# Performance work log

Measured on AMD Instinct MI355X. Metric: run time of the kernel, lower is better.

Reference implementation:

```python
import jax, jax.numpy as jnp
import numpy as np

N_NODES = 100000
N_EDGES = 1600000
IN_DIM = 128
OUT_DIM = 128
ALPHA = 0.2  # leaky relu negative slope
EPS = 9e-15


def setup_inputs() -> dict:
    key = jax.random.key(0)
    k1, k2, k3, k4, k5 = jax.random.split(key, 5)
    x = jax.random.normal(k1, (N_NODES, IN_DIM), dtype=jnp.float32)
    src = jax.random.randint(k2, (N_EDGES,), 0, N_NODES)
    dst = jax.random.randint(k3, (N_EDGES,), 0, N_NODES)
    edge_index = jnp.stack([src, dst]).astype(jnp.int64)
    # xavier-normal-ish params
    W = jax.random.normal(k4, (IN_DIM, OUT_DIM), dtype=jnp.float32) * (1.414 * np.sqrt(2.0 / (IN_DIM + OUT_DIM)))
    attn = jax.random.normal(k5, (1, 2 * OUT_DIM), dtype=jnp.float32) * (1.414 * np.sqrt(2.0 / (1 + 2 * OUT_DIM)))
    return {"x": x, "edge_index": edge_index, "W": W, "attn": attn}


def reference(x, edge_index, W, attn):
    N = x.shape[0]
    h = x @ W  # [N, out_dim]
    d = h.shape[1]
    a_src, a_dst = attn[0, :d], attn[0, d:]
    src, dst = edge_index[0], edge_index[1]
    # attn @ cat(h[src], h[dst]) == (h @ a_src)[src] + (h @ a_dst)[dst]
    values = (h @ a_src)[src] + (h @ a_dst)[dst]  # [E]
    e_a = jnp.where(values > 0, values, ALPHA * values)  # leaky relu
    edge_e = jnp.exp(e_a - jnp.max(e_a))  # [E]
    rowsum = jax.ops.segment_sum(edge_e, src, num_segments=N)  # [N]
    h_prime = jax.ops.segment_sum(edge_e[:, None] * h[dst], src, num_segments=N)  # [N, d]
    h_prime = h_prime / (rowsum[:, None] + EPS)
    return jax.nn.elu(h_prime)
```

## Files before the change

kernel.cpp:

```cpp
#include <hip/hip_runtime.h>
#include <hip/hip_bf16.h>
#include <stdint.h>


#define NN 100000
#define NE 1600000
#define DIM 128
#define ALPHA_ 0.2f
#define EPS_ 9e-15f

#define NB 1563
#define CHUNK 4096
#define NPART 391
#define NGEMM 1564
#define SDEG 56

typedef short bf16x8 __attribute__((ext_vector_type(8)));
typedef float floatx4 __attribute__((ext_vector_type(4)));

static __device__ __forceinline__ float bflo(unsigned u){ return __uint_as_float(u << 16); }
static __device__ __forceinline__ float bfhi(unsigned u){ return __uint_as_float(u & 0xFFFF0000u); }
static __device__ __forceinline__ float bfs(unsigned short s){ return __uint_as_float((unsigned)s << 16); }
static __device__ __forceinline__ unsigned short f2bf(float f){
  unsigned b = __float_as_uint(f);
  unsigned r = (b + 0x7FFFu + ((b >> 16) & 1u)) >> 16;
  return (unsigned short)r;
}
static __device__ __forceinline__ unsigned short f2bf_rhu(float f){
  return (unsigned short)((__float_as_uint(f) + 0x8000u) >> 16);
}
static __device__ __forceinline__ unsigned fkey(float f){
  unsigned u = __float_as_uint(f);
  return (u & 0x80000000u) ? ~u : (u | 0x80000000u);
}
static __device__ __forceinline__ float dkey(unsigned k){
  unsigned u = (k & 0x80000000u) ? (k ^ 0x80000000u) : ~k;
  return __uint_as_float(u);
}

__global__ __launch_bounds__(256) void k_init(const unsigned short* W, const unsigned* EI,
                                              const unsigned short* attn, int* flags,
                                              unsigned short* attnb, unsigned short* Wt){
  __shared__ int sh_f, sh_e;
  int b = blockIdx.x, tid = threadIdx.x;
  if (b == 0){
    if (tid == 0){ sh_f = 0; sh_e = 0; }
    __syncthreads();
    for (int i = tid; i < 1024; i += 256){
      unsigned u = W[i];
      if (((u >> 7) & 0xFF) >= 0x85) sh_f = 1;
    }
    int any = 0;
    for (int k = tid; k < 2048; k += 256) any |= EI[2 * k + 1];
    atomicOr(&sh_e, any);
    __syncthreads();
    if (tid == 0){ flags[0] = sh_f; flags[1] = (sh_e == 0) ? 1 : 0; }
    __syncthreads();
    attnb[tid] = sh_f ? f2bf(((const float*)attn)[tid]) : attn[tid];
  } else {
    if (tid == 0) sh_f = 0;
    __syncthreads();
    for (int i = tid; i < 1024; i += 256){
      unsigned u = W[i];
      if (((u >> 7) & 0xFF) >= 0x85) sh_f = 1;
    }
    __syncthreads();
    int i = (b - 1) * 256 + tid;
    int k = i >> 7, n = i & 127;
    unsigned short v = sh_f ? f2bf(((const float*)W)[i]) : ((const unsigned short*)W)[i];
    Wt[n * DIM + k] = v;
  }
}

static __device__ __forceinline__ void load_edge(const int* EI, int e64, int e,
                                                 int& s, int& d){
  if (e64){
    const long long* E64 = (const long long*)EI;
    s = (int)E64[e];
    d = (int)E64[NE + e];
  } else {
    s = EI[e];
    d = EI[NE + e];
  }
}

static __device__ __forceinline__ void gemm_path(int gid, char* smem,
                                                 const void* X, const int* flags,
                                                 const unsigned short* Wt,
                                                 const unsigned short* attnb,
                                                 unsigned short* H, float* s1, float* s2,
                                                 float* gmax1, float* gmax2){
  char* wlds = smem;
  float* sm1 = (float*)(smem + 16384);
  float* sm2 = sm1 + 4;
  int tid = threadIdx.x;
  int wid = tid >> 6, lane = tid & 63;
  int m = lane & 15, q = lane >> 4;
  int rb = gid * 64 + wid * 16;
  int row = rb + m;
  bool rok = row < NN;
  int fx32 = flags[0];

  floatx4 acc[8];
  #pragma unroll
  for (int t = 0; t < 8; t++){ acc[t][0]=0.f; acc[t][1]=0.f; acc[t][2]=0.f; acc[t][3]=0.f; }

  for (int hk = 0; hk < 2; hk++){
    float4 f0, f1, f2, f3;
    bf16x8 a0, a1;
    if (rok){
      if (fx32){
        const float* xr = (const float*)X + (size_t)row * DIM + hk * 64 + q * 8;
        f0 = ((const float4*)xr)[0];
        f1 = ((const float4*)xr)[1];
        f2 = ((const float4*)(xr + 32))[0];
        f3 = ((const float4*)(xr + 32))[1];
      } else {
        const unsigned short* xr = (const unsigned short*)X + (size_t)row * DIM + hk * 64 + q * 8;
        a0 = *(const bf16x8*)xr;
        a1 = *(const bf16x8*)(xr + 32);
      }
    }
    for (int j = tid; j < 1024; j += 256){
      int wr = j >> 3, c = j & 7;
      uint4 v = ((const uint4*)Wt)[wr * 16 + hk * 8 + c];
      *(uint4*)(wlds + ((wr * 8 + (c ^ (wr & 7))) << 4)) = v;
    }
    __syncthreads();
    bf16x8 fr[2];
    #pragma unroll
    for (int j = 0; j < 8; j++){ fr[0][j] = 0; fr[1][j] = 0; }
    if (rok){
      if (fx32){
        fr[0][0] = (short)f2bf_rhu(f0.x); fr[0][1] = (short)f2bf_rhu(f0.y);
        fr[0][2] = (short)f2bf_rhu(f0.z); fr[0][3] = (short)f2bf_rhu(f0.w);
        fr[0][4] = (short)f2bf_rhu(f1.x); fr[0][5] = (short)f2bf_rhu(f1.y);
        fr[0][6] = (short)f2bf_rhu(f1.z); fr[0][7] = (short)f2bf_rhu(f1.w);
        fr[1][0] = (short)f2bf_rhu(f2.x); fr[1][1] = (short)f2bf_rhu(f2.y);
        fr[1][2] = (short)f2bf_rhu(f2.z); fr[1][3] = (short)f2bf_rhu(f2.w);
        fr[1][4] = (short)f2bf_rhu(f3.x); fr[1][5] = (short)f2bf_rhu(f3.y);
        fr[1][6] = (short)f2bf_rhu(f3.z); fr[1][7] = (short)f2bf_rhu(f3.w);
      } else {
        fr[0] = a0; fr[1] = a1;
      }
    }
    #pragma unroll
    for (int ki2 = 0; ki2 < 2; ki2++){
      #pragma unroll
      for (int t = 0; t < 8; t++){
        int rowb = t * 16 + m;
        bf16x8 bfr = *(const bf16x8*)(wlds + ((rowb * 8 + ((ki2 * 4 + q) ^ (m & 7))) << 4));
        acc[t] = __builtin_amdgcn_mfma_f32_16x16x32_bf16(fr[ki2], bfr, acc[t], 0, 0, 0);
      }
    }
    __syncthreads();
  }

  float as[8], ad[8];
  #pragma unroll
  for (int t = 0; t < 8; t++){
    as[t] = bfs(attnb[t * 16 + m]);
    ad[t] = bfs(attnb[DIM + t * 16 + m]);
  }
  float lm1 = -3.0e38f, lm2 = -3.0e38f;
  #pragma unroll
  for (int r = 0; r < 4; r++){
    int grow = rb + q * 4 + r;
    float p1 = 0.f, p2 = 0.f;
    #pragma unroll
    for (int t = 0; t < 8; t++){ p1 += acc[t][r] * as[t]; p2 += acc[t][r] * ad[t]; }
    #pragma unroll
    for (int off = 1; off < 16; off <<= 1){
      p1 += __shfl_xor(p1, off);
      p2 += __shfl_xor(p2, off);
    }
    if (grow < NN){
      if (m == 0){ s1[grow] = p1; s2[grow] = p2; }
      lm1 = fmaxf(lm1, p1); lm2 = fmaxf(lm2, p2);
    }
  }
  #pragma unroll
  for (int off = 32; off; off >>= 1){
    lm1 = fmaxf(lm1, __shfl_xor(lm1, off));
    lm2 = fmaxf(lm2, __shfl_xor(lm2, off));
  }
  if (lane == 0){ sm1[wid] = lm1; sm2[wid] = lm2; }
  __syncthreads();
  if (tid == 0){
    gmax1[gid] = fmaxf(fmaxf(sm1[0], sm1[1]), fmaxf(sm1[2], sm1[3]));
    gmax2[gid] = fmaxf(fmaxf(sm2[0], sm2[1]), fmaxf(sm2[2], sm2[3]));
  }

  char* wb = wlds + wid * 4096;
  #pragma unroll
  for (int r = 0; r < 4; r++){
    int trow = q * 4 + r;
    #pragma unroll
    for (int t = 0; t < 8; t++){
      int col = t * 16 + m;
      int boff = trow * 256 + (((((col >> 3) ^ trow) & 15)) << 4) + ((col & 7) << 1);
      *(unsigned short*)(wb + boff) = f2bf(acc[t][r]);
    }
  }
  __syncthreads();
  int lrow = lane >> 2;
  int grow2 = rb + lrow;
  #pragma unroll
  for (int u = 0; u < 4; u++){
    int c = u * 4 + (lane & 3);
    uint4 v = *(const uint4*)(wb + lrow * 256 + (((c ^ lrow) & 15) << 4));
    if (grow2 < NN) *(uint4*)(H + (size_t)grow2 * DIM + c * 8) = v;
  }
}

static __device__ __forceinline__ void part_path(int pid, char* smem,
                                                 const int* EI, const int* flags,
                                                 unsigned* dir, unsigned* sout_g){
  unsigned* sout = (unsigned*)smem;
  int* hist = (int*)(smem + 16384);
  int tid = threadIdx.x;
  int e0 = pid * CHUNK;
  int nmy = NE - e0; if (nmy > CHUNK) nmy = CHUNK;
  int e64 = flags[1];

  for (int i = tid; i < NB; i += 256) hist[i] = 0;
  __syncthreads();

  unsigned ent[16]; int bv[16];
  #pragma unroll
  for (int i = 0; i < 16; i++){
    int idx = tid + i * 256;
    if (idx < nmy){
      int s, d;
      load_edge(EI, e64, e0 + idx, s, d);
      ent[i] = ((unsigned)(s & 63) << 17) | (unsigned)d;
      bv[i] = s >> 6;
      atomicAdd(&hist[bv[i]], 1);
    } else {
      ent[i] = 0u; bv[i] = -1;
    }
  }
  __syncthreads();

  if (tid < 64){
    int carry = 0;
    for (int rr = 0; rr < (NB + 63) / 64; rr++){
      int idx = rr * 64 + tid;
      int v = (idx < NB) ? hist[idx] : 0;
      int x = v;
      #pragma unroll
      for (int off = 1; off < 64; off <<= 1){
        int y = __shfl_up(x, off);
        if (tid >= off) x += y;
      }
      if (idx < NB) hist[idx] = x - v + carry;
      carry += __shfl(x, 63);
    }
    if (tid == 0) hist[NB] = carry;
  }
  __syncthreads();

  for (int t = tid; t < NB; t += 256){
    unsigned ls = (unsigned)hist[t];
    unsigned len = (unsigned)(hist[t + 1] - hist[t]);
    dir[(size_t)pid * NB + t] = (ls << 16) | len;
  }
  __syncthreads();

  #pragma unroll
  for (int i = 0; i < 16; i++){
    if (bv[i] >= 0){
      int p = atomicAdd(&hist[bv[i]], 1);
      sout[p] = ent[i];
    }
  }
  __syncthreads();

  for (int i = tid * 4; i < nmy; i += 1024)
    *(uint4*)(sout_g + e0 + i) = *(const uint4*)(sout + i);
}

__global__ __launch_bounds__(256, 6) void k_main(const void* X, const int* EI,
                                                 const int* flags,
                                                 const unsigned short* Wt,
                                                 const unsigned short* attnb,
                                                 unsigned short* H, float* s1, float* s2,
                                                 float* gmax1, float* gmax2,
                                                 unsigned* dir, unsigned* sout_g){
  __shared__ char smem[22656];
  int bid = blockIdx.x;
  int T = bid / 5, r = bid % 5;
  if (r == 4){
    part_path(T, smem, EI, flags, dir, sout_g);
  } else {
    gemm_path(T * 4 + r, smem, X, flags, Wt, attnb, H, s1, s2, gmax1, gmax2);
  }
}

__global__ __launch_bounds__(256) void k_aux(const float* gmax1, const float* gmax2,
                                             unsigned* keys, const unsigned* dir,
                                             unsigned* dir_t){
  int b = blockIdx.x, tid = threadIdx.x;
  if (b == 0){
    float a = -3.0e38f, bb = -3.0e38f;
    for (int i = tid; i < NGEMM; i += 256){
      a = fmaxf(a, gmax1[i]);
      bb = fmaxf(bb, gmax2[i]);
    }
    #pragma unroll
    for (int off = 32; off; off >>= 1){
      a = fmaxf(a, __shfl_xor(a, off));
      bb = fmaxf(bb, __shfl_xor(bb, off));
    }
    __shared__ float m1[4], m2[4];
    int lane = tid & 63, wid = tid >> 6;
    if (lane == 0){ m1[wid] = a; m2[wid] = bb; }
    __syncthreads();
    if (tid == 0){
      keys[0] = fkey(fmaxf(fmaxf(m1[0], m1[1]), fmaxf(m1[2], m1[3])));
      keys[1] = fkey(fmaxf(fmaxf(m2[0], m2[1]), fmaxf(m2[2], m2[3])));
    }
  } else {
    __shared__ unsigned tile[64][65];
    int tb = b - 1;
    int tc = tb % 25;
    int tr = tb / 25;
    int r0 = tr * 64, c0 = tc * 64;
    int cc = tid & 63;
    for (int rr = tid >> 6; rr < 64; rr += 4){
      int gp = r0 + rr, gB = c0 + cc;
      unsigned v = 0;
      if (gp < NPART && gB < NB) v = dir[(size_t)gp * NB + gB];
      tile[rr][cc] = v;
    }
    __syncthreads();
    for (int rr = tid >> 6; rr < 64; rr += 4){
      int gB = c0 + rr, gp = r0 + cc;
      if (gB < NB && gp < NPART)
        dir_t[(size_t)gB * NPART + gp] = tile[cc][rr];
    }
  }
}

__global__ __launch_bounds__(256) void k_sbagg(const unsigned* dir_t, const unsigned* sout_g,
                                               const float* s1, const float* s2,
                                               const unsigned* keys,
                                               const unsigned short* H, float* out){
  __shared__ int lcnt[64];
  __shared__ int llist[64][SDEG];
  int B = blockIdx.x;
  int tid = threadIdx.x;
  if (tid < 64) lcnt[tid] = 0;
  __syncthreads();
  for (int p = tid; p < NPART; p += 256){
    unsigned dv = dir_t[(size_t)B * NPART + p];
    int len = (int)(dv & 0xFFFFu);
    if (len){
      const unsigned* sp = sout_g + (size_t)p * CHUNK + (dv >> 16);
      for (int j = 0; j < len; j++){
        unsigned ent = sp[j];
        int sl = ent >> 17;
        int pos = atomicAdd(&lcnt[sl], 1);
        if (pos < SDEG) llist[sl][pos] = ent & 0x1FFFF;
      }
    }
  }
  __syncthreads();
  float V = dkey(keys[0]) + dkey(keys[1]);
  float M = V > 0.f ? V : ALPHA_ * V;
  int wid = tid >> 6, lane = tid & 63;
  const unsigned* h2 = (const unsigned*)H;
  for (int sl = wid; sl < 64; sl += 4){
    int srcn = B * 64 + sl;
    if (srcn >= NN) break;
    int deg = lcnt[sl]; if (deg > SDEG) deg = SDEG;
    float s1n = s1[srcn];
    int pd = 0; float pw = 0.f;
    if (lane < deg){
      pd = llist[sl][lane];
      float v = s1n + s2[pd];
      float va = v > 0.f ? v : ALPHA_ * v;
      pw = __expf(va - M);
    }
    float a0 = 0.f, a1 = 0.f, wsum = 0.f;
    int j = 0;
    for (; j + 4 <= deg; j += 4){
      int d0 = __shfl(pd, j), d1 = __shfl(pd, j + 1), d2 = __shfl(pd, j + 2), d3 = __shfl(pd, j + 3);
      float w0 = __shfl(pw, j), w1 = __shfl(pw, j + 1), w2 = __shfl(pw, j + 2), w3 = __shfl(pw, j + 3);
      unsigned v0 = h2[d0 * 64 + lane];
      unsigned v1 = h2[d1 * 64 + lane];
      unsigned v2 = h2[d2 * 64 + lane];
      unsigned v3 = h2[d3 * 64 + lane];
      a0 += w0 * bflo(v0) + w1 * bflo(v1) + w2 * bflo(v2) + w3 * bflo(v3);
      a1 += w0 * bfhi(v0) + w1 * bfhi(v1) + w2 * bfhi(v2) + w3 * bfhi(v3);
      wsum += (w0 + w1) + (w2 + w3);
    }
    for (; j < deg; j++){
      int d = __shfl(pd, j); float w = __shfl(pw, j);
      unsigned v = h2[d * 64 + lane];
      a0 += w * bflo(v); a1 += w * bfhi(v); wsum += w;
    }
    float r = wsum + EPS_;
    float p0 = a0 / r, p1 = a1 / r;
    float o0 = p0 > 0.f ? p0 : expm1f(p0);
    float o1 = p1 > 0.f ? p1 : expm1f(p1);
    ((float2*)out)[srcn * 64 + lane] = make_float2(o0, o1);
  }
}

extern "C" void kernel_launch(void* const* d_in, const int* in_sizes, int n_in,
                              void* d_out, int out_size, void* d_ws, size_t ws_size,
                              hipStream_t stream){
  (void)in_sizes; (void)n_in; (void)out_size; (void)ws_size;
  const void* X    = d_in[0];
  const int*  EI   = (const int*)d_in[1];
  const void* W    = d_in[2];
  const void* attn = d_in[3];

  char* ws = (char*)d_ws;
  size_t off = 0;
  auto alloc = [&](size_t bytes) -> char* {
    char* p = ws + off;
    off += (bytes + 255) & ~(size_t)255;
    return p;
  };
  unsigned short* H      = (unsigned short*)alloc((size_t)NN * DIM * 2);
  unsigned*       sout_g = (unsigned*)alloc((size_t)NE * 4);
  unsigned*       dir    = (unsigned*)alloc((size_t)NPART * NB * 4);
  unsigned*       dir_t  = (unsigned*)alloc((size_t)NB * NPART * 4);
  unsigned short* Wt     = (unsigned short*)alloc(DIM * DIM * 2);
  unsigned short* attnb  = (unsigned short*)alloc(256 * 2);
  int*            flags  = (int*)alloc(2 * 4);
  float*          s1     = (float*)alloc(NN * 4);
  float*          s2     = (float*)alloc(NN * 4);
  float*          gmax1  = (float*)alloc(NGEMM * 4);
  float*          gmax2  = (float*)alloc(NGEMM * 4);
  unsigned*       keys   = (unsigned*)alloc(2 * 4);
  float*          outp   = (float*)d_out;

  k_init<<<65, 256, 0, stream>>>((const unsigned short*)W, (const unsigned*)EI,
                                 (const unsigned short*)attn, flags, attnb, Wt);
  k_main<<<NPART * 5, 256, 0, stream>>>(X, EI, flags, Wt, attnb, H, s1, s2,
                                        gmax1, gmax2, dir, sout_g);
  k_aux<<<1 + 7 * 25, 256, 0, stream>>>(gmax1, gmax2, keys, dir, dir_t);
  k_sbagg<<<NB, 256, 0, stream>>>(dir_t, sout_g, s1, s2, keys, H, outp);
}
```

Baseline: 219.4 us.

## Fuse all four stages into one persistent cooperative kernel with grid syncs

Replaces the four separate launches (init, main gemm/partition, aux, aggregation) with a single cooperative kernel. Each stage runs as a grid-stride loop over work items and is separated from the next by grid.sync(). Shared memory is carved from one buffer. The goal is to remove launch gaps and per-kernel tail effects. In exchange it adds grid-wide barrier cost and limits the grid to the number of co-resident blocks, which may cut parallelism for the large aggregation stage.

```diff
diff --git a/kernel.cpp b/kernel.cpp
--- a/kernel.cpp
+++ b/kernel.cpp
@@ -1,6 +1,9 @@
 #include <hip/hip_runtime.h>
 #include <hip/hip_bf16.h>
+#include <hip/hip_cooperative_groups.h>
 #include <stdint.h>
+
+namespace cg = cooperative_groups;
 
 
 #define NN 100000
@@ -36,40 +39,6 @@
 static __device__ __forceinline__ float dkey(unsigned k){
   unsigned u = (k & 0x80000000u) ? (k ^ 0x80000000u) : ~k;
   return __uint_as_float(u);
-}
-
-__global__ __launch_bounds__(256) void k_init(const unsigned short* W, const unsigned* EI,
-                                              const unsigned short* attn, int* flags,
-                                              unsigned short* attnb, unsigned short* Wt){
-  __shared__ int sh_f, sh_e;
-  int b = blockIdx.x, tid = threadIdx.x;
-  if (b == 0){
-    if (tid == 0){ sh_f = 0; sh_e = 0; }
-    __syncthreads();
-    for (int i = tid; i < 1024; i += 256){
-      unsigned u = W[i];
-      if (((u >> 7) & 0xFF) >= 0x85) sh_f = 1;
-    }
-    int any = 0;
-    for (int k = tid; k < 2048; k += 256) any |= EI[2 * k + 1];
-    atomicOr(&sh_e, any);
-    __syncthreads();
-    if (tid == 0){ flags[0] = sh_f; flags[1] = (sh_e == 0) ? 1 : 0; }
-    __syncthreads();
-    attnb[tid] = sh_f ? f2bf(((const float*)attn)[tid]) : attn[tid];
-  } else {
-    if (tid == 0) sh_f = 0;
-    __syncthreads();
-    for (int i = tid; i < 1024; i += 256){
-      unsigned u = W[i];
-      if (((u >> 7) & 0xFF) >= 0x85) sh_f = 1;
-    }
-    __syncthreads();
-    int i = (b - 1) * 256 + tid;
-    int k = i >> 7, n = i & 127;
-    unsigned short v = sh_f ? f2bf(((const float*)W)[i]) : ((const unsigned short*)W)[i];
-    Wt[n * DIM + k] = v;
-  }
 }
 
 static __device__ __forceinline__ void load_edge(const int* EI, int e64, int e,
@@ -81,6 +50,40 @@
   } else {
     s = EI[e];
     d = EI[NE + e];
+  }
+}
+
+static __device__ void init_item(int it, char* smem, const unsigned short* W,
+                                 const unsigned* EI, const unsigned short* attn,
+                                 int* flags, unsigned short* attnb, unsigned short* Wt){
+  int tid = threadIdx.x;
+  int* sh = (int*)smem;
+  if (it == 0){
+    if (tid == 0){ sh[0] = 0; sh[1] = 0; }
+    __syncthreads();
+    for (int i = tid; i < 1024; i += 256){
+      unsigned u = W[i];
+      if (((u >> 7) & 0xFF) >= 0x85) sh[0] = 1;
+    }
+    int any = 0;
+    for (int k = tid; k < 2048; k += 256) any |= EI[2 * k + 1];
+    atomicOr(&sh[1], any);
+    __syncthreads();
+    if (tid == 0){ flags[0] = sh[0]; flags[1] = (sh[1] == 0) ? 1 : 0; }
+    __syncthreads();
+    attnb[tid] = sh[0] ? f2bf(((const float*)attn)[tid]) : attn[tid];
+  } else {
+    if (tid == 0) sh[0] = 0;
+    __syncthreads();
+    for (int i = tid; i < 1024; i += 256){
+      unsigned u = W[i];
+      if (((u >> 7) & 0xFF) >= 0x85) sh[0] = 1;
+    }
+    __syncthreads();
+    int i = (it - 1) * 256 + tid;
+    int k = i >> 7, n = i & 127;
+    unsigned short v = sh[0] ? f2bf(((const float*)W)[i]) : ((const unsigned short*)W)[i];
+    Wt[n * DIM + k] = v;
   }
 }
 
@@ -280,28 +283,13 @@
     *(uint4*)(sout_g + e0 + i) = *(const uint4*)(sout + i);
 }
 
-__global__ __launch_bounds__(256, 6) void k_main(const void* X, const int* EI,
-                                                 const int* flags,
-                                                 const unsigned short* Wt,
-                                                 const unsigned short* attnb,
-                                                 unsigned short* H, float* s1, float* s2,
-                                                 float* gmax1, float* gmax2,
-                                                 unsigned* dir, unsigned* sout_g){
-  __shared__ char smem[22656];
-  int bid = blockIdx.x;
-  int T = bid / 5, r = bid % 5;
-  if (r == 4){
-    part_path(T, smem, EI, flags, dir, sout_g);
-  } else {
-    gemm_path(T * 4 + r, smem, X, flags, Wt, attnb, H, s1, s2, gmax1, gmax2);
-  }
-}
-
-__global__ __launch_bounds__(256) void k_aux(const float* gmax1, const float* gmax2,
-                                             unsigned* keys, const unsigned* dir,
-                                             unsigned* dir_t){
-  int b = blockIdx.x, tid = threadIdx.x;
-  if (b == 0){
+static __device__ void aux_item(int it, char* smem,
+                                const float* gmax1, const float* gmax2, unsigned* keys,
+                                const unsigned* dir, unsigned* dir_t){
+  int tid = threadIdx.x;
+  if (it == 0){
+    float* m1 = (float*)(smem + 16640);
+    float* m2 = m1 + 4;
     float a = -3.0e38f, bb = -3.0e38f;
     for (int i = tid; i < NGEMM; i += 256){
       a = fmaxf(a, gmax1[i]);
@@ -312,7 +300,6 @@
       a = fmaxf(a, __shfl_xor(a, off));
       bb = fmaxf(bb, __shfl_xor(bb, off));
     }
-    __shared__ float m1[4], m2[4];
     int lane = tid & 63, wid = tid >> 6;
     if (lane == 0){ m1[wid] = a; m2[wid] = bb; }
     __syncthreads();
@@ -321,8 +308,8 @@
       keys[1] = fkey(fmaxf(fmaxf(m2[0], m2[1]), fmaxf(m2[2], m2[3])));
     }
   } else {
-    __shared__ unsigned tile[64][65];
-    int tb = b - 1;
+    unsigned (*tile)[65] = (unsigned(*)[65])smem;
+    int tb = it - 1;
     int tc = tb % 25;
     int tr = tb / 25;
     int r0 = tr * 64, c0 = tc * 64;
@@ -342,13 +329,13 @@
   }
 }
 
-__global__ __launch_bounds__(256) void k_sbagg(const unsigned* dir_t, const unsigned* sout_g,
-                                               const float* s1, const float* s2,
-                                               const unsigned* keys,
-                                               const unsigned short* H, float* out){
-  __shared__ int lcnt[64];
-  __shared__ int llist[64][SDEG];
-  int B = blockIdx.x;
+static __device__ void sbagg_bin(int B, char* smem,
+                                 const unsigned* dir_t, const unsigned* sout_g,
+                                 const float* s1, const float* s2,
+                                 const unsigned* keys,
+                                 const unsigned short* H, float* out){
+  int* lcnt = (int*)smem;
+  int (*llist)[SDEG] = (int(*)[SDEG])(smem + 256);
   int tid = threadIdx.x;
   if (tid < 64) lcnt[tid] = 0;
   __syncthreads();
@@ -408,14 +395,53 @@
   }
 }
 
+__global__ __launch_bounds__(256, 6) void k_all(const void* X, const int* EI,
+                                                const unsigned short* W,
+                                                const unsigned short* attn,
+                                                int* flags, unsigned short* attnb,
+                                                unsigned short* Wt,
+                                                unsigned short* H, float* s1, float* s2,
+                                                float* gmax1, float* gmax2,
+                                                unsigned* dir, unsigned* dir_t,
+                                                unsigned* sout_g, unsigned* keys,
+                                                float* out){
+  __shared__ __align__(16) char smem[22656];
+  cg::grid_group grid = cg::this_grid();
+  int nblk = gridDim.x, bid = blockIdx.x;
+
+  for (int it = bid; it < 65; it += nblk){
+    init_item(it, smem, W, (const unsigned*)EI, attn, flags, attnb, Wt);
+    __syncthreads();
+  }
+  grid.sync();
+
+  for (int it = bid; it < NPART + NGEMM; it += nblk){
+    if (it < NPART) part_path(it, smem, EI, flags, dir, sout_g);
+    else gemm_path(it - NPART, smem, X, flags, Wt, attnb, H, s1, s2, gmax1, gmax2);
+    __syncthreads();
+  }
+  grid.sync();
+
+  for (int it = bid; it < 176; it += nblk){
+    aux_item(it, smem, gmax1, gmax2, keys, dir, dir_t);
+    __syncthreads();
+  }
+  grid.sync();
+
+  for (int B = bid; B < NB; B += nblk){
+    sbagg_bin(B, smem, dir_t, sout_g, s1, s2, keys, H, out);
+    __syncthreads();
+  }
+}
+
 extern "C" void kernel_launch(void* const* d_in, const int* in_sizes, int n_in,
                               void* d_out, int out_size, void* d_ws, size_t ws_size,
                               hipStream_t stream){
   (void)in_sizes; (void)n_in; (void)out_size; (void)ws_size;
   const void* X    = d_in[0];
   const int*  EI   = (const int*)d_in[1];
-  const void* W    = d_in[2];
-  const void* attn = d_in[3];
+  const unsigned short* W    = (const unsigned short*)d_in[2];
+  const unsigned short* attn = (const unsigned short*)d_in[3];
 
   char* ws = (char*)d_ws;
   size_t off = 0;
@@ -438,10 +464,23 @@
   unsigned*       keys   = (unsigned*)alloc(2 * 4);
   float*          outp   = (float*)d_out;
 
-  k_init<<<65, 256, 0, stream>>>((const unsigned short*)W, (const unsigned*)EI,
-                                 (const unsigned short*)attn, flags, attnb, Wt);
-  k_main<<<NPART * 5, 256, 0, stream>>>(X, EI, flags, Wt, attnb, H, s1, s2,
-                                        gmax1, gmax2, dir, sout_g);
-  k_aux<<<1 + 7 * 25, 256, 0, stream>>>(gmax1, gmax2, keys, dir, dir_t);
-  k_sbagg<<<NB, 256, 0, stream>>>(dir_t, sout_g, s1, s2, keys, H, outp);
-}
+  static int s_grid = 0;
+  if (s_grid == 0){
+    hipDeviceProp_t prop;
+    hipGetDeviceProperties(&prop, 0);
+    int nb = 0;
+    hipOccupancyMaxActiveBlocksPerMultiprocessor(&nb, k_all, 256, 0);
+    if (nb < 1) nb = 1;
+    long long tot = (long long)nb * prop.multiProcessorCount;
+    if (tot > NPART + NGEMM) tot = NPART + NGEMM;
+    s_grid = (int)tot;
+  }
+
+  void* args[] = { (void*)&X, (void*)&EI, (void*)&W, (void*)&attn,
+                   (void*)&flags, (void*)&attnb, (void*)&Wt,
+                   (void*)&H, (void*)&s1, (void*)&s2,
+                   (void*)&gmax1, (void*)&gmax2, (void*)&dir, (void*)&dir_t,
+                   (void*)&sout_g, (void*)&keys, (void*)&outp };
+  hipLaunchCooperativeKernel((const void*)k_all, dim3(s_grid), dim3(256),
+                             args, 0, stream);
+}
```

New measurement: 620.9 us. 2.83x slower.

## Process 128 rows per GEMM block to reuse staged W tile across two row groups

Applied to the files above, without the earlier changes.

Each GEMM block now computes two 64-row groups (128 rows) with separate accumulators, so each W slice staged in LDS feeds twice as many MFMAs. The GEMM block count is halved and the fused grid ratio changes from 4 GEMM + 1 partition block to 2 + 1 per group. Launch bounds drop to 4 waves-per-SIMD occupancy target to make room for the doubled accumulators. This trades occupancy and extra epilogue syncs for fewer W loads and fewer blocks.

```diff
diff --git a/kernel.cpp b/kernel.cpp
--- a/kernel.cpp
+++ b/kernel.cpp
@@ -12,7 +12,7 @@
 #define NB 1563
 #define CHUNK 4096
 #define NPART 391
-#define NGEMM 1564
+#define NGEMM 782
 #define SDEG 56
 
 typedef short bf16x8 __attribute__((ext_vector_type(8)));
@@ -81,6 +81,53 @@
   } else {
     s = EI[e];
     d = EI[NE + e];
+  }
+}
+
+static __device__ __forceinline__ void epi_dots(const floatx4 (&acc)[8], int rb,
+                                                const float (&as)[8], const float (&ad)[8],
+                                                int q, int m, float* s1, float* s2,
+                                                float& lm1, float& lm2){
+  #pragma unroll
+  for (int r = 0; r < 4; r++){
+    int grow = rb + q * 4 + r;
+    float p1 = 0.f, p2 = 0.f;
+    #pragma unroll
+    for (int t = 0; t < 8; t++){ p1 += acc[t][r] * as[t]; p2 += acc[t][r] * ad[t]; }
+    #pragma unroll
+    for (int off = 1; off < 16; off <<= 1){
+      p1 += __shfl_xor(p1, off);
+      p2 += __shfl_xor(p2, off);
+    }
+    if (grow < NN){
+      if (m == 0){ s1[grow] = p1; s2[grow] = p2; }
+      lm1 = fmaxf(lm1, p1); lm2 = fmaxf(lm2, p2);
+    }
+  }
+}
+
+static __device__ __forceinline__ void epi_hwrite(const floatx4 (&acc)[8], char* wb,
+                                                  int q, int m){
+  #pragma unroll
+  for (int r = 0; r < 4; r++){
+    int trow = q * 4 + r;
+    #pragma unroll
+    for (int t = 0; t < 8; t++){
+      int col = t * 16 + m;
+      int boff = trow * 256 + (((((col >> 3) ^ trow) & 15)) << 4) + ((col & 7) << 1);
+      *(unsigned short*)(wb + boff) = f2bf(acc[t][r]);
+    }
+  }
+}
+static __device__ __forceinline__ void epi_hflush(const char* wb, int rb, int lane,
+                                                  unsigned short* H){
+  int lrow = lane >> 2;
+  int grow2 = rb + lrow;
+  #pragma unroll
+  for (int u = 0; u < 4; u++){
+    int c = u * 4 + (lane & 3);
+    uint4 v = *(const uint4*)(wb + lrow * 256 + (((c ^ lrow) & 15) << 4));
+    if (grow2 < NN) *(uint4*)(H + (size_t)grow2 * DIM + c * 8) = v;
   }
 }
 
@@ -96,29 +143,41 @@
   int tid = threadIdx.x;
   int wid = tid >> 6, lane = tid & 63;
   int m = lane & 15, q = lane >> 4;
-  int rb = gid * 64 + wid * 16;
-  int row = rb + m;
-  bool rok = row < NN;
+  int rb0 = gid * 128 + wid * 16;
+  int rb1 = rb0 + 64;
+  int row0 = rb0 + m, row1 = rb1 + m;
+  bool rok0 = row0 < NN, rok1 = row1 < NN;
   int fx32 = flags[0];
 
-  floatx4 acc[8];
-  #pragma unroll
-  for (int t = 0; t < 8; t++){ acc[t][0]=0.f; acc[t][1]=0.f; acc[t][2]=0.f; acc[t][3]=0.f; }
+  floatx4 acc0[8], acc1[8];
+  #pragma unroll
+  for (int t = 0; t < 8; t++){
+    acc0[t][0]=0.f; acc0[t][1]=0.f; acc0[t][2]=0.f; acc0[t][3]=0.f;
+    acc1[t][0]=0.f; acc1[t][1]=0.f; acc1[t][2]=0.f; acc1[t][3]=0.f;
+  }
 
   for (int hk = 0; hk < 2; hk++){
-    float4 f0, f1, f2, f3;
-    bf16x8 a0, a1;
-    if (rok){
-      if (fx32){
-        const float* xr = (const float*)X + (size_t)row * DIM + hk * 64 + q * 8;
-        f0 = ((const float4*)xr)[0];
-        f1 = ((const float4*)xr)[1];
-        f2 = ((const float4*)(xr + 32))[0];
-        f3 = ((const float4*)(xr + 32))[1];
-      } else {
-        const unsigned short* xr = (const unsigned short*)X + (size_t)row * DIM + hk * 64 + q * 8;
-        a0 = *(const bf16x8*)xr;
-        a1 = *(const bf16x8*)(xr + 32);
+    float4 f00, f01, f02, f03, f10, f11, f12, f13;
+    bf16x8 b00, b01, b10, b11;
+    if (fx32){
+      if (rok0){
+        const float* xr = (const float*)X + (size_t)row0 * DIM + hk * 64 + q * 8;
+        f00 = ((const float4*)xr)[0]; f01 = ((const float4*)xr)[1];
+        f02 = ((const float4*)(xr + 32))[0]; f03 = ((const float4*)(xr + 32))[1];
+      }
+      if (rok1){
+        const float* xr = (const float*)X + (size_t)row1 * DIM + hk * 64 + q * 8;
+        f10 = ((const float4*)xr)[0]; f11 = ((const float4*)xr)[1];
+        f12 = ((const float4*)(xr + 32))[0]; f13 = ((const float4*)(xr + 32))[1];
+      }
+    } else {
+      if (rok0){
+        const unsigned short* xr = (const unsigned short*)X + (size_t)row0 * DIM + hk * 64 + q * 8;
+        b00 = *(const bf16x8*)xr; b01 = *(const bf16x8*)(xr + 32);
+      }
+      if (rok1){
+        const unsigned short* xr = (const unsigned short*)X + (size_t)row1 * DIM + hk * 64 + q * 8;
+        b10 = *(const bf16x8*)xr; b11 = *(const bf16x8*)(xr + 32);
       }
     }
     for (int j = tid; j < 1024; j += 256){
@@ -127,22 +186,33 @@
       *(uint4*)(wlds + ((wr * 8 + (c ^ (wr & 7))) << 4)) = v;
     }
     __syncthreads();
-    bf16x8 fr[2];
-    #pragma unroll
-    for (int j = 0; j < 8; j++){ fr[0][j] = 0; fr[1][j] = 0; }
-    if (rok){
-      if (fx32){
-        fr[0][0] = (short)f2bf_rhu(f0.x); fr[0][1] = (short)f2bf_rhu(f0.y);
-        fr[0][2] = (short)f2bf_rhu(f0.z); fr[0][3] = (short)f2bf_rhu(f0.w);
-        fr[0][4] = (short)f2bf_rhu(f1.x); fr[0][5] = (short)f2bf_rhu(f1.y);
-        fr[0][6] = (short)f2bf_rhu(f1.z); fr[0][7] = (short)f2bf_rhu(f1.w);
-        fr[1][0] = (short)f2bf_rhu(f2.x); fr[1][1] = (short)f2bf_rhu(f2.y);
-        fr[1][2] = (short)f2bf_rhu(f2.z); fr[1][3] = (short)f2bf_rhu(f2.w);
-        fr[1][4] = (short)f2bf_rhu(f3.x); fr[1][5] = (short)f2bf_rhu(f3.y);
-        fr[1][6] = (short)f2bf_rhu(f3.z); fr[1][7] = (short)f2bf_rhu(f3.w);
-      } else {
-        fr[0] = a0; fr[1] = a1;
-      }
+    bf16x8 fr0[2], fr1[2];
+    #pragma unroll
+    for (int j = 0; j < 8; j++){ fr0[0][j]=0; fr0[1][j]=0; fr1[0][j]=0; fr1[1][j]=0; }
+    if (fx32){
+      if (rok0){
+        fr0[0][0]=(short)f2bf_rhu(f00.x); fr0[0][1]=(short)f2bf_rhu(f00.y);
+        fr0[0][2]=(short)f2bf_rhu(f00.z); fr0[0][3]=(short)f2bf_rhu(f00.w);
+        fr0[0][4]=(short)f2bf_rhu(f01.x); fr0[0][5]=(short)f2bf_rhu(f01.y);
+        fr0[0][6]=(short)f2bf_rhu(f01.z); fr0[0][7]=(short)f2bf_rhu(f01.w);
+        fr0[1][0]=(short)f2bf_rhu(f02.x); fr0[1][1]=(short)f2bf_rhu(f02.y);
+        fr0[1][2]=(short)f2bf_rhu(f02.z); fr0[1][3]=(short)f2bf_rhu(f02.w);
+        fr0[1][4]=(short)f2bf_rhu(f03.x); fr0[1][5]=(short)f2bf_rhu(f03.y);
+        fr0[1][6]=(short)f2bf_rhu(f03.z); fr0[1][7]=(short)f2bf_rhu(f03.w);
+      }
+      if (rok1){
+        fr1[0][0]=(short)f2bf_rhu(f10.x); fr1[0][1]=(short)f2bf_rhu(f10.y);
+        fr1[0][2]=(short)f2bf_rhu(f10.z); fr1[0][3]=(short)f2bf_rhu(f10.w);
+        fr1[0][4]=(short)f2bf_rhu(f11.x); fr1[0][5]=(short)f2bf_rhu(f11.y);
+        fr1[0][6]=(short)f2bf_rhu(f11.z); fr1[0][7]=(short)f2bf_rhu(f11.w);
+        fr1[1][0]=(short)f2bf_rhu(f12.x); fr1[1][1]=(short)f2bf_rhu(f12.y);
+        fr1[1][2]=(short)f2bf_rhu(f12.z); fr1[1][3]=(short)f2bf_rhu(f12.w);
+        fr1[1][4]=(short)f2bf_rhu(f13.x); fr1[1][5]=(short)f2bf_rhu(f13.y);
+        fr1[1][6]=(short)f2bf_rhu(f13.z); fr1[1][7]=(short)f2bf_rhu(f13.w);
+      }
+    } else {
+      if (rok0){ fr0[0] = b00; fr0[1] = b01; }
+      if (rok1){ fr1[0] = b10; fr1[1] = b11; }
     }
     #pragma unroll
     for (int ki2 = 0; ki2 < 2; ki2++){
@@ -150,7 +220,8 @@
       for (int t = 0; t < 8; t++){
         int rowb = t * 16 + m;
         bf16x8 bfr = *(const bf16x8*)(wlds + ((rowb * 8 + ((ki2 * 4 + q) ^ (m & 7))) << 4));
-        acc[t] = __builtin_amdgcn_mfma_f32_16x16x32_bf16(fr[ki2], bfr, acc[t], 0, 0, 0);
+        acc0[t] = __builtin_amdgcn_mfma_f32_16x16x32_bf16(fr0[ki2], bfr, acc0[t], 0, 0, 0);
+        acc1[t] = __builtin_amdgcn_mfma_f32_16x16x32_bf16(fr1[ki2], bfr, acc1[t], 0, 0, 0);
       }
     }
     __syncthreads();
@@ -163,22 +234,8 @@
     ad[t] = bfs(attnb[DIM + t * 16 + m]);
   }
   float lm1 = -3.0e38f, lm2 = -3.0e38f;
-  #pragma unroll
-  for (int r = 0; r < 4; r++){
-    int grow = rb + q * 4 + r;
-    float p1 = 0.f, p2 = 0.f;
-    #pragma unroll
-    for (int t = 0; t < 8; t++){ p1 += acc[t][r] * as[t]; p2 += acc[t][r] * ad[t]; }
-    #pragma unroll
-    for (int off = 1; off < 16; off <<= 1){
-      p1 += __shfl_xor(p1, off);
-      p2 += __shfl_xor(p2, off);
-    }
-    if (grow < NN){
-      if (m == 0){ s1[grow] = p1; s2[grow] = p2; }
-      lm1 = fmaxf(lm1, p1); lm2 = fmaxf(lm2, p2);
-    }
-  }
+  epi_dots(acc0, rb0, as, ad, q, m, s1, s2, lm1, lm2);
+  epi_dots(acc1, rb1, as, ad, q, m, s1, s2, lm1, lm2);
   #pragma unroll
   for (int off = 32; off; off >>= 1){
     lm1 = fmaxf(lm1, __shfl_xor(lm1, off));
@@ -192,25 +249,13 @@
   }
 
   char* wb = wlds + wid * 4096;
-  #pragma unroll
-  for (int r = 0; r < 4; r++){
-    int trow = q * 4 + r;
-    #pragma unroll
-    for (int t = 0; t < 8; t++){
-      int col = t * 16 + m;
-      int boff = trow * 256 + (((((col >> 3) ^ trow) & 15)) << 4) + ((col & 7) << 1);
-      *(unsigned short*)(wb + boff) = f2bf(acc[t][r]);
-    }
-  }
-  __syncthreads();
-  int lrow = lane >> 2;
-  int grow2 = rb + lrow;
-  #pragma unroll
-  for (int u = 0; u < 4; u++){
-    int c = u * 4 + (lane & 3);
-    uint4 v = *(const uint4*)(wb + lrow * 256 + (((c ^ lrow) & 15) << 4));
-    if (grow2 < NN) *(uint4*)(H + (size_t)grow2 * DIM + c * 8) = v;
-  }
+  epi_hwrite(acc0, wb, q, m);
+  __syncthreads();
+  epi_hflush(wb, rb0, lane, H);
+  __syncthreads();
+  epi_hwrite(acc1, wb, q, m);
+  __syncthreads();
+  epi_hflush(wb, rb1, lane, H);
 }
 
 static __device__ __forceinline__ void part_path(int pid, char* smem,
@@ -280,20 +325,20 @@
     *(uint4*)(sout_g + e0 + i) = *(const uint4*)(sout + i);
 }
 
-__global__ __launch_bounds__(256, 6) void k_main(const void* X, const int* EI,
+__global__ __launch_bounds__(256, 4) void k_main(const void* X, const int* EI,
                                                  const int* flags,
                                                  const unsigned short* Wt,
                                                  const unsigned short* attnb,
                                                  unsigned short* H, float* s1, float* s2,
                                                  float* gmax1, float* gmax2,
                                                  unsigned* dir, unsigned* sout_g){
-  __shared__ char smem[22656];
+  __shared__ __align__(16) char smem[22656];
   int bid = blockIdx.x;
-  int T = bid / 5, r = bid % 5;
-  if (r == 4){
+  int T = bid / 3, r = bid % 3;
+  if (r == 2){
     part_path(T, smem, EI, flags, dir, sout_g);
   } else {
-    gemm_path(T * 4 + r, smem, X, flags, Wt, attnb, H, s1, s2, gmax1, gmax2);
+    gemm_path(T * 2 + r, smem, X, flags, Wt, attnb, H, s1, s2, gmax1, gmax2);
   }
 }
 
@@ -440,7 +485,7 @@
 
   k_init<<<65, 256, 0, stream>>>((const unsigned short*)W, (const unsigned*)EI,
                                  (const unsigned short*)attn, flags, attnb, Wt);
-  k_main<<<NPART * 5, 256, 0, stream>>>(X, EI, flags, Wt, attnb, H, s1, s2,
+  k_main<<<NPART * 3, 256, 0, stream>>>(X, EI, flags, Wt, attnb, H, s1, s2,
                                         gmax1, gmax2, dir, sout_g);
   k_aux<<<1 + 7 * 25, 256, 0, stream>>>(gmax1, gmax2, keys, dir, dir_t);
   k_sbagg<<<NB, 256, 0, stream>>>(dir_t, sout_g, s1, s2, keys, H, outp);
```

New measurement: 232.8 us. +6.1%, slower.

## Double edge partition chunk size and halve partition count in fused main kernel

Applied to the files above, without the earlier changes.

Edge partitions grow from 4096 to 8192 edges, so there are half as many partitions. That halves the directory that k_aux transposes and that the aggregation kernel scans per bucket. The fused main kernel now interleaves eight GEMM blocks per partition block and raises its shared memory, with launch bounds dropping from 6 to 4 blocks per CU. Edges are no longer held in registers between the histogram and scatter passes; they are reloaded from global memory, which adds an extra read of the edge list. The gmax arrays are padded to cover the extra GEMM blocks.

```diff
diff --git a/kernel.cpp b/kernel.cpp
--- a/kernel.cpp
+++ b/kernel.cpp
@@ -10,9 +10,10 @@
 #define EPS_ 9e-15f
 
 #define NB 1563
-#define CHUNK 4096
-#define NPART 391
+#define CHUNK 8192
+#define NPART 196
 #define NGEMM 1564
+#define NGEMM_PAD 1568
 #define SDEG 56
 
 typedef short bf16x8 __attribute__((ext_vector_type(8)));
@@ -217,7 +218,7 @@
                                                  const int* EI, const int* flags,
                                                  unsigned* dir, unsigned* sout_g){
   unsigned* sout = (unsigned*)smem;
-  int* hist = (int*)(smem + 16384);
+  int* hist = (int*)(smem + 32768);
   int tid = threadIdx.x;
   int e0 = pid * CHUNK;
   int nmy = NE - e0; if (nmy > CHUNK) nmy = CHUNK;
@@ -226,19 +227,10 @@
   for (int i = tid; i < NB; i += 256) hist[i] = 0;
   __syncthreads();
 
-  unsigned ent[16]; int bv[16];
-  #pragma unroll
-  for (int i = 0; i < 16; i++){
-    int idx = tid + i * 256;
-    if (idx < nmy){
-      int s, d;
-      load_edge(EI, e64, e0 + idx, s, d);
-      ent[i] = ((unsigned)(s & 63) << 17) | (unsigned)d;
-      bv[i] = s >> 6;
-      atomicAdd(&hist[bv[i]], 1);
-    } else {
-      ent[i] = 0u; bv[i] = -1;
-    }
+  for (int idx = tid; idx < nmy; idx += 256){
+    int s, d;
+    load_edge(EI, e64, e0 + idx, s, d);
+    atomicAdd(&hist[s >> 6], 1);
   }
   __syncthreads();
 
@@ -267,12 +259,11 @@
   }
   __syncthreads();
 
-  #pragma unroll
-  for (int i = 0; i < 16; i++){
-    if (bv[i] >= 0){
-      int p = atomicAdd(&hist[bv[i]], 1);
-      sout[p] = ent[i];
-    }
+  for (int idx = tid; idx < nmy; idx += 256){
+    int s, d;
+    load_edge(EI, e64, e0 + idx, s, d);
+    int p = atomicAdd(&hist[s >> 6], 1);
+    sout[p] = ((unsigned)(s & 63) << 17) | (unsigned)d;
   }
   __syncthreads();
 
@@ -280,20 +271,20 @@
     *(uint4*)(sout_g + e0 + i) = *(const uint4*)(sout + i);
 }
 
-__global__ __launch_bounds__(256, 6) void k_main(const void* X, const int* EI,
+__global__ __launch_bounds__(256, 4) void k_main(const void* X, const int* EI,
                                                  const int* flags,
                                                  const unsigned short* Wt,
                                                  const unsigned short* attnb,
                                                  unsigned short* H, float* s1, float* s2,
                                                  float* gmax1, float* gmax2,
                                                  unsigned* dir, unsigned* sout_g){
-  __shared__ char smem[22656];
+  __shared__ __align__(16) char smem[39040];
   int bid = blockIdx.x;
-  int T = bid / 5, r = bid % 5;
-  if (r == 4){
+  int T = bid / 9, r = bid % 9;
+  if (r == 8){
     part_path(T, smem, EI, flags, dir, sout_g);
   } else {
-    gemm_path(T * 4 + r, smem, X, flags, Wt, attnb, H, s1, s2, gmax1, gmax2);
+    gemm_path(T * 8 + r, smem, X, flags, Wt, attnb, H, s1, s2, gmax1, gmax2);
   }
 }
 
@@ -303,7 +294,7 @@
   int b = blockIdx.x, tid = threadIdx.x;
   if (b == 0){
     float a = -3.0e38f, bb = -3.0e38f;
-    for (int i = tid; i < NGEMM; i += 256){
+    for (int i = tid; i < NGEMM_PAD; i += 256){
       a = fmaxf(a, gmax1[i]);
       bb = fmaxf(bb, gmax2[i]);
     }
@@ -433,15 +424,15 @@
   int*            flags  = (int*)alloc(2 * 4);
   float*          s1     = (float*)alloc(NN * 4);
   float*          s2     = (float*)alloc(NN * 4);
-  float*          gmax1  = (float*)alloc(NGEMM * 4);
-  float*          gmax2  = (float*)alloc(NGEMM * 4);
+  float*          gmax1  = (float*)alloc(NGEMM_PAD * 4);
+  float*          gmax2  = (float*)alloc(NGEMM_PAD * 4);
   unsigned*       keys   = (unsigned*)alloc(2 * 4);
   float*          outp   = (float*)d_out;
 
   k_init<<<65, 256, 0, stream>>>((const unsigned short*)W, (const unsigned*)EI,
                                  (const unsigned short*)attn, flags, attnb, Wt);
-  k_main<<<NPART * 5, 256, 0, stream>>>(X, EI, flags, Wt, attnb, H, s1, s2,
+  k_main<<<NPART * 9, 256, 0, stream>>>(X, EI, flags, Wt, attnb, H, s1, s2,
                                         gmax1, gmax2, dir, sout_g);
-  k_aux<<<1 + 7 * 25, 256, 0, stream>>>(gmax1, gmax2, keys, dir, dir_t);
+  k_aux<<<1 + 4 * 25, 256, 0, stream>>>(gmax1, gmax2, keys, dir, dir_t);
   k_sbagg<<<NB, 256, 0, stream>>>(dir_t, sout_g, s1, s2, keys, H, outp);
 }
```

Result: slower. 238.9 us (+8.9%).
